# Performance work log

Hardware: AMD Instinct MI355X
Metric: run time of the kernel (lower is better)

Reference implementation:

```python
import jax, jax.numpy as jnp
import numpy as np
from functools import partial

B, S, I, H, L = 32, 512, 512, 512, 2  # batch, seq, input, hidden, layers (bidirectional)


def _uniform(key, shape, k):
    return jax.random.uniform(key, shape, jnp.float32, -k, k)


def setup_inputs() -> dict:
    key = jax.random.key(0)
    keys = jax.random.split(key, 1 + 16)
    inp = {"x": jax.random.normal(keys[0], (B, S, I), jnp.float32)}
    k = 1.0 / H
    ki = 1
    for l in range(L):
        in_sz = I if l == 0 else 2 * H
        for d in ("f", "b"):
            inp[f"w_ih_{l}{d}"] = _uniform(keys[ki], (4 * H, in_sz), k); ki += 1
            inp[f"w_hh_{l}{d}"] = _uniform(keys[ki], (4 * H, H), k); ki += 1
            inp[f"b_ih_{l}{d}"] = _uniform(keys[ki], (4 * H,), k); ki += 1
            inp[f"b_hh_{l}{d}"] = _uniform(keys[ki], (4 * H,), k); ki += 1
    return inp


def _lstm_dir(x_sbi, w_ih, w_hh, b_ih, b_hh, reverse):
    # x_sbi: [S,B,in]. Precompute input projection for all timesteps (one big GEMM).
    xp = jnp.einsum('sbi,gi->sbg', x_sbi, w_ih) + b_ih + b_hh  # [S,B,4H]
    h0 = jnp.zeros((x_sbi.shape[1], H), x_sbi.dtype)
    c0 = jnp.zeros_like(h0)

    def step(carry, xg):
        h, c = carry
        gates = xg + h @ w_hh.T
        i, f, g, o = jnp.split(gates, 4, axis=-1)  # pytorch order i,f,g,o
        i = jax.nn.sigmoid(i); f = jax.nn.sigmoid(f)
        g = jnp.tanh(g); o = jax.nn.sigmoid(o)
        c_new = f * c + i * g
        h_new = o * jnp.tanh(c_new)
        return (h_new, c_new), h_new

    (hT, cT), hs = jax.lax.scan(step, (h0, c0), xp, reverse=reverse)
    return hs, hT, cT  # hs in original time order [S,B,H]


def _forward(x, params):
    seq = jnp.transpose(x, (1, 0, 2))  # [S,B,I]
    final_h, final_c = [], []
    for l in range(L):
        hf, hTf, cTf = _lstm_dir(seq, *params[(l, 'f')], reverse=False)
        hb, hTb, cTb = _lstm_dir(seq, *params[(l, 'b')], reverse=True)
        seq = jnp.concatenate([hf, hb], axis=-1)  # [S,B,2H]
        final_h += [hTf, hTb]; final_c += [cTf, cTb]
    out = jnp.transpose(seq, (1, 0, 2))  # [B,S,2H]
    return out, (jnp.stack(final_h, 0), jnp.stack(final_c, 0))


def reference(x,
              w_ih_0f, w_hh_0f, b_ih_0f, b_hh_0f,
              w_ih_0b, w_hh_0b, b_ih_0b, b_hh_0b,
              w_ih_1f, w_hh_1f, b_ih_1f, b_hh_1f,
              w_ih_1b, w_hh_1b, b_ih_1b, b_hh_1b):
    params = {
        (0, 'f'): (w_ih_0f, w_hh_0f, b_ih_0f, b_hh_0f),
        (0, 'b'): (w_ih_0b, w_hh_0b, b_ih_0b, b_hh_0b),
        (1, 'f'): (w_ih_1f, w_hh_1f, b_ih_1f, b_hh_1f),
        (1, 'b'): (w_ih_1b, w_hh_1b, b_ih_1b, b_hh_1b),
    }
    return _forward(x, params)
```

## Files before the change

### kernel.cpp

```cpp
#include <hip/hip_runtime.h>

#define BB 32
#define SS 512
#define II 512
#define HH 512
#define GG 2048

typedef unsigned short u16;
typedef unsigned int   u32;
typedef unsigned long long u64;

typedef __attribute__((ext_vector_type(8))) short bf16x8;
typedef __attribute__((ext_vector_type(4))) float f32x4;

__device__ __forceinline__ float b2f(u16 h) {
    return __uint_as_float(((u32)h) << 16);
}
__device__ __forceinline__ u16 f2b(float f) {
    u32 u = __float_as_uint(f);
    u32 r = (u + 0x7FFFu + ((u >> 16) & 1u)) >> 16;
    return (u16)r;
}

#ifndef __has_builtin
#define __has_builtin(x) 0
#endif
#if __has_builtin(__builtin_amdgcn_global_load_lds)
#define HAVE_GLL 1
#else
#define HAVE_GLL 0
#endif

typedef __attribute__((address_space(1))) void as1_void;
typedef __attribute__((address_space(3))) void as3_void;

__device__ __forceinline__ void gload16(const void* g, void* l, int lane) {
#if HAVE_GLL
    __builtin_amdgcn_global_load_lds((as1_void*)g, (as3_void*)l, 16, 0, 0);
#else
    *(bf16x8*)((char*)l + lane * 16) = *(const bf16x8*)g;
#endif
}

__global__ void k_convert_x(const float* __restrict__ x, u16* __restrict__ xbf) {
    const int n4 = BB * SS * II / 4;
    for (int e4 = blockIdx.x * blockDim.x + threadIdx.x; e4 < n4;
         e4 += gridDim.x * blockDim.x) {
        int e = e4 * 4;
        int s = e >> 14;
        int b = (e >> 9) & 31;
        int i = e & 511;
        float4 v = *(const float4*)(x + (size_t)b * (SS * II) + (size_t)s * II + i);
        ushort4 o;
        o.x = f2b(v.x); o.y = f2b(v.y); o.z = f2b(v.z); o.w = f2b(v.w);
        *(ushort4*)(xbf + (size_t)s * (BB * II) + (size_t)b * II + i) = o;
    }
}

__global__ void k_cast(const float* __restrict__ src, u16* __restrict__ dst, int n4) {
    for (int e4 = blockIdx.x * blockDim.x + threadIdx.x; e4 < n4;
         e4 += gridDim.x * blockDim.x) {
        float4 v = *(const float4*)(src + (size_t)e4 * 4);
        ushort4 o;
        o.x = f2b(v.x); o.y = f2b(v.y); o.z = f2b(v.z); o.w = f2b(v.w);
        *(ushort4*)(dst + (size_t)e4 * 4) = o;
    }
}

#define BKP 64

__launch_bounds__(256)
__global__ void k_proj(const u16* __restrict__ A,
                       const u16* __restrict__ Wf_, const u16* __restrict__ Wb_,
                       const float* __restrict__ bihf, const float* __restrict__ bhhf,
                       const float* __restrict__ bihb, const float* __restrict__ bhhb,
                       u16* __restrict__ xpf, u16* __restrict__ xpb,
                       int K) {
    const int dir = blockIdx.z;
    const u16* Wm = dir ? Wb_ : Wf_;
    const float* bih = dir ? bihb : bihf;
    const float* bhh = dir ? bhhb : bhhf;
    u16* xp = dir ? xpb : xpf;

    __shared__ __align__(16) u16 As[128 * BKP];
    __shared__ __align__(16) u16 Bs[128 * BKP];

    const int t    = threadIdx.x;
    const int lane = t & 63;
    const int w    = t >> 6;
    const int wm   = w >> 1, wn = w & 1;
    const int m0   = blockIdx.x * 128;
    const int n0   = blockIdx.y * 128;

    f32x4 acc[4][4] = {};

    for (int kt = 0; kt < K; kt += BKP) {
        #pragma unroll
        for (int i = 0; i < 4; ++i) {
            int c   = (w * 4 + i) * 64 + lane;
            int row = c >> 3;
            int lc  = (c & 7) ^ (row & 7);
            int gk  = kt + lc * 8;
            gload16(A  + (size_t)(m0 + row) * K + gk, (char*)As + (w * 4 + i) * 1024, lane);
            gload16(Wm + (size_t)(n0 + row) * K + gk, (char*)Bs + (w * 4 + i) * 1024, lane);
        }
        __syncthreads();

        #pragma unroll
        for (int ks = 0; ks < 2; ++ks) {
            const int kc = ks * 4 + (lane >> 4);
            bf16x8 af[4], bfr[4];
            #pragma unroll
            for (int mi = 0; mi < 4; ++mi) {
                int row = wm * 64 + mi * 16 + (lane & 15);
                af[mi] = *(const bf16x8*)&As[row * BKP + ((kc ^ (row & 7)) << 3)];
            }
            #pragma unroll
            for (int ni = 0; ni < 4; ++ni) {
                int row = wn * 64 + ni * 16 + (lane & 15);
                bfr[ni] = *(const bf16x8*)&Bs[row * BKP + ((kc ^ (row & 7)) << 3)];
            }
            #pragma unroll
            for (int mi = 0; mi < 4; ++mi)
                #pragma unroll
                for (int ni = 0; ni < 4; ++ni)
                    acc[mi][ni] = __builtin_amdgcn_mfma_f32_16x16x32_bf16(
                        af[mi], bfr[ni], acc[mi][ni], 0, 0, 0);
        }
        __syncthreads();
    }

    #pragma unroll
    for (int ni = 0; ni < 4; ++ni) {
        int n = n0 + wn * 64 + ni * 16 + (lane & 15);
        float bias = bih[n] + bhh[n];
        #pragma unroll
        for (int mi = 0; mi < 4; ++mi) {
            #pragma unroll
            for (int r = 0; r < 4; ++r) {
                int m = m0 + wm * 64 + mi * 16 + (lane >> 4) * 4 + r;
                xp[(size_t)m * GG + n] = f2b(acc[mi][ni][r] + bias);
            }
        }
    }
}

__launch_bounds__(256)
__global__ void k_rec(const u16* __restrict__ xpf, const u16* __restrict__ xpb,
                      const float* __restrict__ whf, const float* __restrict__ whb,
                      u64* __restrict__ Hd,
                      u16* __restrict__ hs0,
                      float* __restrict__ out,
                      float* __restrict__ fin,
                      int layer) {
    const int bid  = blockIdx.x;
    const int dir  = bid >> 5;
    const int wg   = bid & 31;
    const int j0   = wg * 16;
    const u16*  xp = dir ? xpb : xpf;
    const float* W = dir ? whb : whf;

    const int t    = threadIdx.x;
    const int lane = t & 63;
    const int g    = t >> 6;

    __shared__ __align__(16) u16 Wfr[64 * 64 * 8];
    __shared__ __align__(16) u16 hl[32 * 512];
    __shared__ float xq[32 * 65];
    __shared__ float gates[4 * 32 * 18];

    for (int it = 0; it < 16; ++it) {
        int task = it * 256 + t;
        int l    = task & 63;
        int blk  = task >> 6;
        int gg   = blk >> 4;
        int kt   = blk & 15;
        const float* src = W + (size_t)(gg * 512 + j0 + (l & 15)) * 512
                             + kt * 32 + (l >> 4) * 8;
        float4 v0 = *(const float4*)src;
        float4 v1 = *(const float4*)(src + 4);
        union { bf16x8 v; u16 a[8]; } u;
        u.a[0] = f2b(v0.x); u.a[1] = f2b(v0.y); u.a[2] = f2b(v0.z); u.a[3] = f2b(v0.w);
        u.a[4] = f2b(v1.x); u.a[5] = f2b(v1.y); u.a[6] = f2b(v1.z); u.a[7] = f2b(v1.w);
        *(bf16x8*)&Wfr[task * 8] = u.v;
    }
    __syncthreads();

    float creg[4] = {0.f, 0.f, 0.f, 0.f};
    const int eb = t >> 2;
    const int ej = t & 3;

    const int sc_c   = t >> 2;
    const int sc_sub = (t & 3) * 4;

    for (int s = 0; s < SS; ++s) {
        const int sa = dir ? (SS - 1 - s) : s;

        if (t < 128) {
            int b = t & 31, gq = t >> 5;
            const u16* xsrc = xp + (size_t)(sa * 32 + b) * GG + gq * 512 + j0;
            bf16x8 v0 = *(const bf16x8*)xsrc;
            bf16x8 v1 = *(const bf16x8*)(xsrc + 8);
            #pragma unroll
            for (int i = 0; i < 8; ++i) {
                xq[b * 65 + gq * 16 + i]     = b2f((u16)v0[i]);
                xq[b * 65 + gq * 16 + 8 + i] = b2f((u16)v1[i]);
            }
        }

        if (s > 0) {
            const u64* Hrd = Hd + ((size_t)((s & 1) * 2 + dir)) * (32 * 256);
            const u32 tgt = (u32)((layer << 10) | s);
            for (;;) {
                u64 w = __hip_atomic_load(Hrd + t, __ATOMIC_RELAXED,
                                          __HIP_MEMORY_SCOPE_AGENT);
                bool f = (((u32)w & 0xffffu) == tgt) &&
                         ((((u32)(w >> 32)) & 0xffffu) == tgt);
                if (__all(f)) break;
            }
            u64 v[32];
            for (;;) {
                #pragma unroll
                for (int i = 0; i < 32; ++i)
                    v[i] = __hip_atomic_load(Hrd + i * 256 + t, __ATOMIC_RELAXED,
                                             __HIP_MEMORY_SCOPE_AGENT);
                bool ok = true;
                #pragma unroll
                for (int i = 0; i < 32; ++i) {
                    ok = ok && (((u32)v[i] & 0xffffu) == tgt);
                    ok = ok && ((((u32)(v[i] >> 32)) & 0xffffu) == tgt);
                }
                if (__all(ok)) break;
            }
            #pragma unroll
            for (int i = 0; i < 32; ++i) {
                u32 two = ((u32)(v[i] >> 16) & 0xffffu) | (((u32)(v[i] >> 48)) << 16);
                int off = i * 1024 + ((sc_c ^ (i & 7)) << 4) + sc_sub;
                *(u32*)((char*)hl + off) = two;
            }
        } else {
            #pragma unroll
            for (int i = 0; i < 32; ++i) {
                int off = i * 1024 + ((sc_c ^ (i & 7)) << 4) + sc_sub;
                *(u32*)((char*)hl + off) = 0u;
            }
        }
        __syncthreads();

        {
            f32x4 acc0 = {0.f, 0.f, 0.f, 0.f}, acc1 = {0.f, 0.f, 0.f, 0.f};
            const int b0 = lane & 15, q = lane >> 4;
            #pragma unroll
            for (int kt = 0; kt < 16; ++kt) {
                int pc = ((kt << 2) + q) ^ (b0 & 7);
                bf16x8 a0 = *(const bf16x8*)&hl[b0 * 512 + pc * 8];
                bf16x8 a1 = *(const bf16x8*)&hl[(b0 + 16) * 512 + pc * 8];
                bf16x8 Bv = *(const bf16x8*)&Wfr[((g * 16 + kt) * 64 + lane) * 8];
                acc0 = __builtin_amdgcn_mfma_f32_16x16x32_bf16(a0, Bv, acc0, 0, 0, 0);
                acc1 = __builtin_amdgcn_mfma_f32_16x16x32_bf16(a1, Bv, acc1, 0, 0, 0);
            }
            #pragma unroll
            for (int r = 0; r < 4; ++r) {
                gates[g * 576 + (q * 4 + r) * 18 + b0]      = acc0[r];
                gates[g * 576 + (16 + q * 4 + r) * 18 + b0] = acc1[r];
            }
        }
        __syncthreads();

        if (t < 128) {
            float hv4[4], cv4[4];
            #pragma unroll
            for (int k = 0; k < 4; ++k) {
                int jj = ej * 4 + k;
                float gi = xq[eb * 65 +      jj] + gates[0 * 576 + eb * 18 + jj];
                float gf = xq[eb * 65 + 16 + jj] + gates[1 * 576 + eb * 18 + jj];
                float gg = xq[eb * 65 + 32 + jj] + gates[2 * 576 + eb * 18 + jj];
                float go = xq[eb * 65 + 48 + jj] + gates[3 * 576 + eb * 18 + jj];
                float ig = 1.f / (1.f + __expf(-gi));
                float fg = 1.f / (1.f + __expf(-gf));
                float gt = tanhf(gg);
                float og = 1.f / (1.f + __expf(-go));
                float c  = fg * creg[k] + ig * gt;
                float h  = og * tanhf(c);
                creg[k] = c; cv4[k] = c; hv4[k] = h;
            }
            u64* Hwr = Hd + ((size_t)(((s + 1) & 1) * 2 + dir)) * (32 * 256);
            const u32 pst = (u32)((layer << 10) | (s + 1));
            u32 w0 = ((u32)f2b(hv4[0]) << 16) | pst;
            u32 w1 = ((u32)f2b(hv4[1]) << 16) | pst;
            u32 w2 = ((u32)f2b(hv4[2]) << 16) | pst;
            u32 w3 = ((u32)f2b(hv4[3]) << 16) | pst;
            u64* dst = Hwr + eb * 256 + ((j0 + ej * 4) >> 1);
            __hip_atomic_store(dst,     (u64)w0 | ((u64)w1 << 32),
                               __ATOMIC_RELAXED, __HIP_MEMORY_SCOPE_AGENT);
            __hip_atomic_store(dst + 1, (u64)w2 | ((u64)w3 << 32),
                               __ATOMIC_RELAXED, __HIP_MEMORY_SCOPE_AGENT);

            union { u64 q; u16 a[4]; } ho;
            #pragma unroll
            for (int k = 0; k < 4; ++k) ho.a[k] = f2b(hv4[k]);
            if (layer == 0) {
                *(u64*)(hs0 + (size_t)sa * (BB * 1024) + (size_t)eb * 1024
                        + dir * 512 + j0 + ej * 4) = ho.q;
            } else {
                *(float4*)(out + (size_t)eb * (SS * 1024) + (size_t)sa * 1024
                           + dir * 512 + j0 + ej * 4) =
                    make_float4(hv4[0], hv4[1], hv4[2], hv4[3]);
            }
            if (s == SS - 1) {
                int sl = layer * 2 + dir;
                *(float4*)(fin + (size_t)sl * (32 * 512) + eb * 512 + j0 + ej * 4) =
                    make_float4(hv4[0], hv4[1], hv4[2], hv4[3]);
                *(float4*)(fin + 65536 + (size_t)sl * (32 * 512) + eb * 512 + j0 + ej * 4) =
                    make_float4(cv4[0], cv4[1], cv4[2], cv4[3]);
            }
        }
        __syncthreads();
    }
}

#define OFF_XBF   ((size_t)0)
#define OFF_HS0   ((size_t)16777216)
#define OFF_XPF   ((size_t)50331648)
#define OFF_XPB   ((size_t)117440512)
#define OFF_WIH0F ((size_t)184549376)
#define OFF_WIH0B ((size_t)186646528)
#define OFF_WIH1F ((size_t)188743680)
#define OFF_WIH1B ((size_t)192937984)
#define OFF_HST   ((size_t)197132288)

extern "C" void kernel_launch(void* const* d_in, const int* in_sizes, int n_in,
                              void* d_out, int out_size, void* d_ws, size_t ws_size,
                              hipStream_t stream) {
    const float* x      = (const float*)d_in[0];
    const float* wih0f  = (const float*)d_in[1];
    const float* whh0f  = (const float*)d_in[2];
    const float* bih0f  = (const float*)d_in[3];
    const float* bhh0f  = (const float*)d_in[4];
    const float* wih0b  = (const float*)d_in[5];
    const float* whh0b  = (const float*)d_in[6];
    const float* bih0b  = (const float*)d_in[7];
    const float* bhh0b  = (const float*)d_in[8];
    const float* wih1f  = (const float*)d_in[9];
    const float* whh1f  = (const float*)d_in[10];
    const float* bih1f  = (const float*)d_in[11];
    const float* bhh1f  = (const float*)d_in[12];
    const float* wih1b  = (const float*)d_in[13];
    const float* whh1b  = (const float*)d_in[14];
    const float* bih1b  = (const float*)d_in[15];
    const float* bhh1b  = (const float*)d_in[16];

    float* out = (float*)d_out;
    char* ws = (char*)d_ws;

    u16* xbf    = (u16*)(ws + OFF_XBF);
    u16* hs0    = (u16*)(ws + OFF_HS0);
    u16* xpf    = (u16*)(ws + OFF_XPF);
    u16* xpb    = (u16*)(ws + OFF_XPB);
    u16* bwih0f = (u16*)(ws + OFF_WIH0F);
    u16* bwih0b = (u16*)(ws + OFF_WIH0B);
    u16* bwih1f = (u16*)(ws + OFF_WIH1F);
    u16* bwih1b = (u16*)(ws + OFF_WIH1B);
    u64* Hd     = (u64*)(ws + OFF_HST);
    float* fin  = out + 16777216;

    k_convert_x<<<1024, 256, 0, stream>>>(x, xbf);
    k_cast<<<512, 256, 0, stream>>>(wih0f, bwih0f, 2048 * 512 / 4);
    k_cast<<<512, 256, 0, stream>>>(wih0b, bwih0b, 2048 * 512 / 4);
    k_cast<<<512, 256, 0, stream>>>(wih1f, bwih1f, 2048 * 1024 / 4);
    k_cast<<<512, 256, 0, stream>>>(wih1b, bwih1b, 2048 * 1024 / 4);

    hipMemsetAsync(ws + OFF_HST, 0, 262144, stream);

    k_proj<<<dim3(128, 16, 2), 256, 0, stream>>>(
        xbf, bwih0f, bwih0b, bih0f, bhh0f, bih0b, bhh0b, xpf, xpb, 512);
    k_rec<<<64, 256, 0, stream>>>(xpf, xpb, whh0f, whh0b, Hd,
                                  hs0, nullptr, fin, 0);

    k_proj<<<dim3(128, 16, 2), 256, 0, stream>>>(
        hs0, bwih1f, bwih1b, bih1f, bhh1f, bih1b, bhh1b, xpf, xpb, 1024);
    k_rec<<<64, 256, 0, stream>>>(xpf, xpb, whh1f, whh1b, Hd,
                                  nullptr, out, fin, 1);
}
```

Before: 5.243 ms.

## Hold recurrent weights in registers and halve recurrence workgroups to 32

```diff
diff --git a/kernel.cpp b/kernel.cpp
--- a/kernel.cpp
+++ b/kernel.cpp
@@ -145,7 +145,7 @@
     }
 }
 
-__launch_bounds__(256)
+__launch_bounds__(256, 1)
 __global__ void k_rec(const u16* __restrict__ xpf, const u16* __restrict__ xpb,
                       const float* __restrict__ whf, const float* __restrict__ whb,
                       u64* __restrict__ Hd,
@@ -154,9 +154,9 @@
                       float* __restrict__ fin,
                       int layer) {
     const int bid  = blockIdx.x;
-    const int dir  = bid >> 5;
-    const int wg   = bid & 31;
-    const int j0   = wg * 16;
+    const int dir  = bid >> 4;
+    const int wg   = bid & 15;
+    const int j0   = wg * 32;
     const u16*  xp = dir ? xpb : xpf;
     const float* W = dir ? whb : whf;
 
@@ -164,31 +164,29 @@
     const int lane = t & 63;
     const int g    = t >> 6;
 
-    __shared__ __align__(16) u16 Wfr[64 * 64 * 8];
     __shared__ __align__(16) u16 hl[32 * 512];
-    __shared__ float xq[32 * 65];
-    __shared__ float gates[4 * 32 * 18];
-
-    for (int it = 0; it < 16; ++it) {
-        int task = it * 256 + t;
-        int l    = task & 63;
-        int blk  = task >> 6;
-        int gg   = blk >> 4;
-        int kt   = blk & 15;
-        const float* src = W + (size_t)(gg * 512 + j0 + (l & 15)) * 512
-                             + kt * 32 + (l >> 4) * 8;
-        float4 v0 = *(const float4*)src;
-        float4 v1 = *(const float4*)(src + 4);
-        union { bf16x8 v; u16 a[8]; } u;
-        u.a[0] = f2b(v0.x); u.a[1] = f2b(v0.y); u.a[2] = f2b(v0.z); u.a[3] = f2b(v0.w);
-        u.a[4] = f2b(v1.x); u.a[5] = f2b(v1.y); u.a[6] = f2b(v1.z); u.a[7] = f2b(v1.w);
-        *(bf16x8*)&Wfr[task * 8] = u.v;
-    }
-    __syncthreads();
+    __shared__ float xq[32 * 129];
+    __shared__ float gates[4 * 32 * 33];
+
+    bf16x8 Bfr[2][16];
+    #pragma unroll
+    for (int nb = 0; nb < 2; ++nb) {
+        #pragma unroll
+        for (int kt = 0; kt < 16; ++kt) {
+            const float* src = W + (size_t)(g * 512 + j0 + nb * 16 + (lane & 15)) * 512
+                                 + kt * 32 + (lane >> 4) * 8;
+            float4 v0 = *(const float4*)src;
+            float4 v1 = *(const float4*)(src + 4);
+            union { bf16x8 v; u16 a[8]; } u;
+            u.a[0] = f2b(v0.x); u.a[1] = f2b(v0.y); u.a[2] = f2b(v0.z); u.a[3] = f2b(v0.w);
+            u.a[4] = f2b(v1.x); u.a[5] = f2b(v1.y); u.a[6] = f2b(v1.z); u.a[7] = f2b(v1.w);
+            Bfr[nb][kt] = u.v;
+        }
+    }
 
     float creg[4] = {0.f, 0.f, 0.f, 0.f};
-    const int eb = t >> 2;
-    const int ej = t & 3;
+    const int eb = t >> 3;
+    const int ec = t & 7;
 
     const int sc_c   = t >> 2;
     const int sc_sub = (t & 3) * 4;
@@ -196,45 +194,43 @@
     for (int s = 0; s < SS; ++s) {
         const int sa = dir ? (SS - 1 - s) : s;
 
-        if (t < 128) {
-            int b = t & 31, gq = t >> 5;
-            const u16* xsrc = xp + (size_t)(sa * 32 + b) * GG + gq * 512 + j0;
+        {
+            int b = t >> 3, seg = t & 7;
+            const u16* xsrc = xp + (size_t)(sa * 32 + b) * GG
+                              + (seg >> 1) * 512 + j0 + (seg & 1) * 16;
             bf16x8 v0 = *(const bf16x8*)xsrc;
             bf16x8 v1 = *(const bf16x8*)(xsrc + 8);
+            float* xdst = &xq[b * 129 + (seg >> 1) * 32 + (seg & 1) * 16];
             #pragma unroll
             for (int i = 0; i < 8; ++i) {
-                xq[b * 65 + gq * 16 + i]     = b2f((u16)v0[i]);
-                xq[b * 65 + gq * 16 + 8 + i] = b2f((u16)v1[i]);
+                xdst[i]     = b2f((u16)v0[i]);
+                xdst[8 + i] = b2f((u16)v1[i]);
             }
         }
 
         if (s > 0) {
             const u64* Hrd = Hd + ((size_t)((s & 1) * 2 + dir)) * (32 * 256);
             const u32 tgt = (u32)((layer << 10) | s);
-            for (;;) {
-                u64 w = __hip_atomic_load(Hrd + t, __ATOMIC_RELAXED,
-                                          __HIP_MEMORY_SCOPE_AGENT);
-                bool f = (((u32)w & 0xffffu) == tgt) &&
-                         ((((u32)(w >> 32)) & 0xffffu) == tgt);
-                if (__all(f)) break;
-            }
             u64 v[32];
+            u32 pend = 0xffffffffu;
             for (;;) {
                 #pragma unroll
-                for (int i = 0; i < 32; ++i)
-                    v[i] = __hip_atomic_load(Hrd + i * 256 + t, __ATOMIC_RELAXED,
-                                             __HIP_MEMORY_SCOPE_AGENT);
-                bool ok = true;
-                #pragma unroll
                 for (int i = 0; i < 32; ++i) {
-                    ok = ok && (((u32)v[i] & 0xffffu) == tgt);
-                    ok = ok && ((((u32)(v[i] >> 32)) & 0xffffu) == tgt);
+                    if (pend & (1u << i)) {
+                        u64 w = __hip_atomic_load(Hrd + i * 256 + t, __ATOMIC_RELAXED,
+                                                  __HIP_MEMORY_SCOPE_AGENT);
+                        if ((((u32)w & 0xffffu) == tgt) &&
+                            (((u32)(w >> 32) & 0xffffu) == tgt)) {
+                            v[i] = w;
+                            pend &= ~(1u << i);
+                        }
+                    }
                 }
-                if (__all(ok)) break;
+                if (__all(pend == 0)) break;
             }
             #pragma unroll
             for (int i = 0; i < 32; ++i) {
-                u32 two = ((u32)(v[i] >> 16) & 0xffffu) | (((u32)(v[i] >> 48)) << 16);
+                u32 two = (u32)((v[i] >> 16) & 0xffffu) | ((u32)(v[i] >> 48) << 16);
                 int off = i * 1024 + ((sc_c ^ (i & 7)) << 4) + sc_sub;
                 *(u32*)((char*)hl + off) = two;
             }
@@ -248,34 +244,43 @@
         __syncthreads();
 
         {
-            f32x4 acc0 = {0.f, 0.f, 0.f, 0.f}, acc1 = {0.f, 0.f, 0.f, 0.f};
+            f32x4 acc[2][2];
+            #pragma unroll
+            for (int mi = 0; mi < 2; ++mi)
+                #pragma unroll
+                for (int nb = 0; nb < 2; ++nb)
+                    acc[mi][nb] = (f32x4){0.f, 0.f, 0.f, 0.f};
             const int b0 = lane & 15, q = lane >> 4;
             #pragma unroll
             for (int kt = 0; kt < 16; ++kt) {
                 int pc = ((kt << 2) + q) ^ (b0 & 7);
                 bf16x8 a0 = *(const bf16x8*)&hl[b0 * 512 + pc * 8];
                 bf16x8 a1 = *(const bf16x8*)&hl[(b0 + 16) * 512 + pc * 8];
-                bf16x8 Bv = *(const bf16x8*)&Wfr[((g * 16 + kt) * 64 + lane) * 8];
-                acc0 = __builtin_amdgcn_mfma_f32_16x16x32_bf16(a0, Bv, acc0, 0, 0, 0);
-                acc1 = __builtin_amdgcn_mfma_f32_16x16x32_bf16(a1, Bv, acc1, 0, 0, 0);
-            }
-            #pragma unroll
-            for (int r = 0; r < 4; ++r) {
-                gates[g * 576 + (q * 4 + r) * 18 + b0]      = acc0[r];
-                gates[g * 576 + (16 + q * 4 + r) * 18 + b0] = acc1[r];
-            }
-        }
-        __syncthreads();
-
-        if (t < 128) {
+                acc[0][0] = __builtin_amdgcn_mfma_f32_16x16x32_bf16(a0, Bfr[0][kt], acc[0][0], 0, 0, 0);
+                acc[0][1] = __builtin_amdgcn_mfma_f32_16x16x32_bf16(a0, Bfr[1][kt], acc[0][1], 0, 0, 0);
+                acc[1][0] = __builtin_amdgcn_mfma_f32_16x16x32_bf16(a1, Bfr[0][kt], acc[1][0], 0, 0, 0);
+                acc[1][1] = __builtin_amdgcn_mfma_f32_16x16x32_bf16(a1, Bfr[1][kt], acc[1][1], 0, 0, 0);
+            }
+            #pragma unroll
+            for (int mi = 0; mi < 2; ++mi)
+                #pragma unroll
+                for (int nb = 0; nb < 2; ++nb)
+                    #pragma unroll
+                    for (int r = 0; r < 4; ++r)
+                        gates[g * 1056 + (mi * 16 + q * 4 + r) * 33 + nb * 16 + b0]
+                            = acc[mi][nb][r];
+        }
+        __syncthreads();
+
+        {
             float hv4[4], cv4[4];
             #pragma unroll
             for (int k = 0; k < 4; ++k) {
-                int jj = ej * 4 + k;
-                float gi = xq[eb * 65 +      jj] + gates[0 * 576 + eb * 18 + jj];
-                float gf = xq[eb * 65 + 16 + jj] + gates[1 * 576 + eb * 18 + jj];
-                float gg = xq[eb * 65 + 32 + jj] + gates[2 * 576 + eb * 18 + jj];
-                float go = xq[eb * 65 + 48 + jj] + gates[3 * 576 + eb * 18 + jj];
+                int jj = ec * 4 + k;
+                float gi = xq[eb * 129 +      jj] + gates[0 * 1056 + eb * 33 + jj];
+                float gf = xq[eb * 129 + 32 + jj] + gates[1 * 1056 + eb * 33 + jj];
+                float gg = xq[eb * 129 + 64 + jj] + gates[2 * 1056 + eb * 33 + jj];
+                float go = xq[eb * 129 + 96 + jj] + gates[3 * 1056 + eb * 33 + jj];
                 float ig = 1.f / (1.f + __expf(-gi));
                 float fg = 1.f / (1.f + __expf(-gf));
                 float gt = tanhf(gg);
@@ -290,7 +295,7 @@
             u32 w1 = ((u32)f2b(hv4[1]) << 16) | pst;
             u32 w2 = ((u32)f2b(hv4[2]) << 16) | pst;
             u32 w3 = ((u32)f2b(hv4[3]) << 16) | pst;
-            u64* dst = Hwr + eb * 256 + ((j0 + ej * 4) >> 1);
+            u64* dst = Hwr + eb * 256 + ((j0 + ec * 4) >> 1);
             __hip_atomic_store(dst,     (u64)w0 | ((u64)w1 << 32),
                                __ATOMIC_RELAXED, __HIP_MEMORY_SCOPE_AGENT);
             __hip_atomic_store(dst + 1, (u64)w2 | ((u64)w3 << 32),
@@ -301,17 +306,17 @@
             for (int k = 0; k < 4; ++k) ho.a[k] = f2b(hv4[k]);
             if (layer == 0) {
                 *(u64*)(hs0 + (size_t)sa * (BB * 1024) + (size_t)eb * 1024
-                        + dir * 512 + j0 + ej * 4) = ho.q;
+                        + dir * 512 + j0 + ec * 4) = ho.q;
             } else {
                 *(float4*)(out + (size_t)eb * (SS * 1024) + (size_t)sa * 1024
-                           + dir * 512 + j0 + ej * 4) =
+                           + dir * 512 + j0 + ec * 4) =
                     make_float4(hv4[0], hv4[1], hv4[2], hv4[3]);
             }
             if (s == SS - 1) {
                 int sl = layer * 2 + dir;
-                *(float4*)(fin + (size_t)sl * (32 * 512) + eb * 512 + j0 + ej * 4) =
+                *(float4*)(fin + (size_t)sl * (32 * 512) + eb * 512 + j0 + ec * 4) =
                     make_float4(hv4[0], hv4[1], hv4[2], hv4[3]);
-                *(float4*)(fin + 65536 + (size_t)sl * (32 * 512) + eb * 512 + j0 + ej * 4) =
+                *(float4*)(fin + 65536 + (size_t)sl * (32 * 512) + eb * 512 + j0 + ec * 4) =
                     make_float4(cv4[0], cv4[1], cv4[2], cv4[3]);
             }
         }
@@ -374,11 +379,11 @@
 
     k_proj<<<dim3(128, 16, 2), 256, 0, stream>>>(
         xbf, bwih0f, bwih0b, bih0f, bhh0f, bih0b, bhh0b, xpf, xpb, 512);
-    k_rec<<<64, 256, 0, stream>>>(xpf, xpb, whh0f, whh0b, Hd,
+    k_rec<<<32, 256, 0, stream>>>(xpf, xpb, whh0f, whh0b, Hd,
                                   hs0, nullptr, fin, 0);
 
     k_proj<<<dim3(128, 16, 2), 256, 0, stream>>>(
         hs0, bwih1f, bwih1b, bih1f, bhh1f, bih1b, bhh1b, xpf, xpb, 1024);
-    k_rec<<<64, 256, 0, stream>>>(xpf, xpb, whh1f, whh1b, Hd,
+    k_rec<<<32, 256, 0, stream>>>(xpf, xpb, whh1f, whh1b, Hd,
                                   nullptr, out, fin, 1);
 }
```

Measured after the change: 12.55 ms. 139% more time.

## Replace step barrier with per-k-tile LDS counters and prefetch hidden state loads

Applied to the files above, without the earlier changes.

```diff
diff --git a/kernel.cpp b/kernel.cpp
--- a/kernel.cpp
+++ b/kernel.cpp
@@ -168,6 +168,7 @@
     __shared__ __align__(16) u16 hl[32 * 512];
     __shared__ float xq[32 * 65];
     __shared__ float gates[4 * 32 * 18];
+    __shared__ u32 ktdone[16];
 
     for (int it = 0; it < 16; ++it) {
         int task = it * 256 + t;
@@ -184,6 +185,7 @@
         u.a[4] = f2b(v1.x); u.a[5] = f2b(v1.y); u.a[6] = f2b(v1.z); u.a[7] = f2b(v1.w);
         *(bf16x8*)&Wfr[task * 8] = u.v;
     }
+    if (t < 16) ktdone[t] = 0u;
     __syncthreads();
 
     float creg[4] = {0.f, 0.f, 0.f, 0.f};
@@ -195,6 +197,16 @@
 
     for (int s = 0; s < SS; ++s) {
         const int sa = dir ? (SS - 1 - s) : s;
+
+        u64 w[32];
+        const u64* Hrd = Hd + ((size_t)((s & 1) * 2 + dir)) * (32 * 256);
+        const u32 tgt = (u32)((layer << 10) | s);
+        if (s > 0) {
+            #pragma unroll
+            for (int i = 0; i < 32; ++i)
+                w[i] = __hip_atomic_load(Hrd + i * 256 + t, __ATOMIC_RELAXED,
+                                         __HIP_MEMORY_SCOPE_AGENT);
+        }
 
         if (t < 128) {
             int b = t & 31, gq = t >> 5;
@@ -209,32 +221,22 @@
         }
 
         if (s > 0) {
-            const u64* Hrd = Hd + ((size_t)((s & 1) * 2 + dir)) * (32 * 256);
-            const u32 tgt = (u32)((layer << 10) | s);
             for (;;) {
-                u64 w = __hip_atomic_load(Hrd + t, __ATOMIC_RELAXED,
-                                          __HIP_MEMORY_SCOPE_AGENT);
-                bool f = (((u32)w & 0xffffu) == tgt) &&
-                         ((((u32)(w >> 32)) & 0xffffu) == tgt);
-                if (__all(f)) break;
-            }
-            u64 v[32];
-            for (;;) {
-                #pragma unroll
-                for (int i = 0; i < 32; ++i)
-                    v[i] = __hip_atomic_load(Hrd + i * 256 + t, __ATOMIC_RELAXED,
-                                             __HIP_MEMORY_SCOPE_AGENT);
                 bool ok = true;
                 #pragma unroll
                 for (int i = 0; i < 32; ++i) {
-                    ok = ok && (((u32)v[i] & 0xffffu) == tgt);
-                    ok = ok && ((((u32)(v[i] >> 32)) & 0xffffu) == tgt);
+                    ok = ok && (((u32)w[i] & 0xffffu) == tgt)
+                            && ((((u32)(w[i] >> 32)) & 0xffffu) == tgt);
                 }
-                if (__all(ok)) break;
+                if (ok) break;
+                #pragma unroll
+                for (int i = 0; i < 32; ++i)
+                    w[i] = __hip_atomic_load(Hrd + i * 256 + t, __ATOMIC_RELAXED,
+                                             __HIP_MEMORY_SCOPE_AGENT);
             }
             #pragma unroll
             for (int i = 0; i < 32; ++i) {
-                u32 two = ((u32)(v[i] >> 16) & 0xffffu) | (((u32)(v[i] >> 48)) << 16);
+                u32 two = (u32)((w[i] >> 16) & 0xffffu) | ((u32)(w[i] >> 48) << 16);
                 int off = i * 1024 + ((sc_c ^ (i & 7)) << 4) + sc_sub;
                 *(u32*)((char*)hl + off) = two;
             }
@@ -245,13 +247,22 @@
                 *(u32*)((char*)hl + off) = 0u;
             }
         }
-        __syncthreads();
+        asm volatile("s_waitcnt lgkmcnt(0)" ::: "memory");
+        atomicAdd(&ktdone[t >> 4], 1u);
 
         {
             f32x4 acc0 = {0.f, 0.f, 0.f, 0.f}, acc1 = {0.f, 0.f, 0.f, 0.f};
             const int b0 = lane & 15, q = lane >> 4;
-            #pragma unroll
-            for (int kt = 0; kt < 16; ++kt) {
+            const u32 kneed = 16u * (u32)(s + 1);
+            #pragma unroll
+            for (int kk = 0; kk < 16; ++kk) {
+                const int kt = (g * 4 + kk) & 15;
+                while (__hip_atomic_load(&ktdone[kt], __ATOMIC_RELAXED,
+                                         __HIP_MEMORY_SCOPE_WORKGROUP) < kneed) {
+                    __builtin_amdgcn_s_sleep(1);
+                }
+                asm volatile("" ::: "memory");
+                __builtin_amdgcn_sched_barrier(0);
                 int pc = ((kt << 2) + q) ^ (b0 & 7);
                 bf16x8 a0 = *(const bf16x8*)&hl[b0 * 512 + pc * 8];
                 bf16x8 a1 = *(const bf16x8*)&hl[(b0 + 16) * 512 + pc * 8];
```

Result: slower. 7.923 ms (+51.1%).

## Double the recurrent workgroup to 512 threads and prefetch next-step hidden state

Applied to the files above, without the earlier changes.

```diff
diff --git a/kernel.cpp b/kernel.cpp
--- a/kernel.cpp
+++ b/kernel.cpp
@@ -145,7 +145,7 @@
     }
 }
 
-__launch_bounds__(256)
+__launch_bounds__(512, 1)
 __global__ void k_rec(const u16* __restrict__ xpf, const u16* __restrict__ xpb,
                       const float* __restrict__ whf, const float* __restrict__ whb,
                       u64* __restrict__ Hd,
@@ -162,15 +162,17 @@
 
     const int t    = threadIdx.x;
     const int lane = t & 63;
-    const int g    = t >> 6;
+    const int wv   = t >> 6;
+    const int g    = wv & 3;
+    const int m    = wv >> 2;
 
     __shared__ __align__(16) u16 Wfr[64 * 64 * 8];
     __shared__ __align__(16) u16 hl[32 * 512];
-    __shared__ float xq[32 * 65];
+    __shared__ float xq[2][32 * 65];
     __shared__ float gates[4 * 32 * 18];
 
-    for (int it = 0; it < 16; ++it) {
-        int task = it * 256 + t;
+    for (int it = 0; it < 8; ++it) {
+        int task = it * 512 + t;
         int l    = task & 63;
         int blk  = task >> 6;
         int gg   = blk >> 4;
@@ -186,136 +188,119 @@
     }
     __syncthreads();
 
-    float creg[4] = {0.f, 0.f, 0.f, 0.f};
-    const int eb = t >> 2;
-    const int ej = t & 3;
-
-    const int sc_c   = t >> 2;
-    const int sc_sub = (t & 3) * 4;
+    const int wd   = t & 255;
+    const int r0   = (t >> 8) * 16;
+    const int sc_c   = wd >> 2;
+    const int sc_sub = (wd & 3) * 4;
+
+    const int eb = t >> 4;
+    const int ej = t & 15;
+    float creg = 0.f;
+
+    u64 w[16];
 
     for (int s = 0; s < SS; ++s) {
         const int sa = dir ? (SS - 1 - s) : s;
 
-        if (t < 128) {
-            int b = t & 31, gq = t >> 5;
-            const u16* xsrc = xp + (size_t)(sa * 32 + b) * GG + gq * 512 + j0;
+        if (t < 256) {
+            int b = t & 31, seg = t >> 5;
+            int gq = seg >> 1, hf = seg & 1;
+            const u16* xsrc = xp + (size_t)(sa * 32 + b) * GG + gq * 512 + j0 + hf * 8;
             bf16x8 v0 = *(const bf16x8*)xsrc;
-            bf16x8 v1 = *(const bf16x8*)(xsrc + 8);
-            #pragma unroll
-            for (int i = 0; i < 8; ++i) {
-                xq[b * 65 + gq * 16 + i]     = b2f((u16)v0[i]);
-                xq[b * 65 + gq * 16 + 8 + i] = b2f((u16)v1[i]);
-            }
+            float* xdst = &xq[s & 1][b * 65 + gq * 16 + hf * 8];
+            #pragma unroll
+            for (int i = 0; i < 8; ++i) xdst[i] = b2f((u16)v0[i]);
         }
 
         if (s > 0) {
             const u64* Hrd = Hd + ((size_t)((s & 1) * 2 + dir)) * (32 * 256);
             const u32 tgt = (u32)((layer << 10) | s);
             for (;;) {
-                u64 w = __hip_atomic_load(Hrd + t, __ATOMIC_RELAXED,
-                                          __HIP_MEMORY_SCOPE_AGENT);
-                bool f = (((u32)w & 0xffffu) == tgt) &&
-                         ((((u32)(w >> 32)) & 0xffffu) == tgt);
-                if (__all(f)) break;
-            }
-            u64 v[32];
-            for (;;) {
-                #pragma unroll
-                for (int i = 0; i < 32; ++i)
-                    v[i] = __hip_atomic_load(Hrd + i * 256 + t, __ATOMIC_RELAXED,
-                                             __HIP_MEMORY_SCOPE_AGENT);
                 bool ok = true;
                 #pragma unroll
-                for (int i = 0; i < 32; ++i) {
-                    ok = ok && (((u32)v[i] & 0xffffu) == tgt);
-                    ok = ok && ((((u32)(v[i] >> 32)) & 0xffffu) == tgt);
+                for (int i = 0; i < 16; ++i) {
+                    ok = ok && (((u32)w[i] & 0xffffu) == tgt)
+                            && ((((u32)(w[i] >> 32)) & 0xffffu) == tgt);
                 }
-                if (__all(ok)) break;
-            }
-            #pragma unroll
-            for (int i = 0; i < 32; ++i) {
-                u32 two = ((u32)(v[i] >> 16) & 0xffffu) | (((u32)(v[i] >> 48)) << 16);
-                int off = i * 1024 + ((sc_c ^ (i & 7)) << 4) + sc_sub;
+                if (ok) break;
+                #pragma unroll
+                for (int i = 0; i < 16; ++i)
+                    w[i] = __hip_atomic_load(Hrd + (r0 + i) * 256 + wd,
+                                             __ATOMIC_RELAXED, __HIP_MEMORY_SCOPE_AGENT);
+            }
+            #pragma unroll
+            for (int i = 0; i < 16; ++i) {
+                int r = r0 + i;
+                u32 two = (u32)((w[i] >> 16) & 0xffffu) | ((u32)(w[i] >> 48) << 16);
+                int off = r * 1024 + ((sc_c ^ (r & 7)) << 4) + sc_sub;
                 *(u32*)((char*)hl + off) = two;
             }
         } else {
             #pragma unroll
-            for (int i = 0; i < 32; ++i) {
-                int off = i * 1024 + ((sc_c ^ (i & 7)) << 4) + sc_sub;
+            for (int i = 0; i < 16; ++i) {
+                int r = r0 + i;
+                int off = r * 1024 + ((sc_c ^ (r & 7)) << 4) + sc_sub;
                 *(u32*)((char*)hl + off) = 0u;
             }
         }
         __syncthreads();
 
         {
-            f32x4 acc0 = {0.f, 0.f, 0.f, 0.f}, acc1 = {0.f, 0.f, 0.f, 0.f};
+            f32x4 acc = {0.f, 0.f, 0.f, 0.f};
             const int b0 = lane & 15, q = lane >> 4;
             #pragma unroll
             for (int kt = 0; kt < 16; ++kt) {
                 int pc = ((kt << 2) + q) ^ (b0 & 7);
-                bf16x8 a0 = *(const bf16x8*)&hl[b0 * 512 + pc * 8];
-                bf16x8 a1 = *(const bf16x8*)&hl[(b0 + 16) * 512 + pc * 8];
+                bf16x8 a0 = *(const bf16x8*)&hl[(b0 + m * 16) * 512 + pc * 8];
                 bf16x8 Bv = *(const bf16x8*)&Wfr[((g * 16 + kt) * 64 + lane) * 8];
-                acc0 = __builtin_amdgcn_mfma_f32_16x16x32_bf16(a0, Bv, acc0, 0, 0, 0);
-                acc1 = __builtin_amdgcn_mfma_f32_16x16x32_bf16(a1, Bv, acc1, 0, 0, 0);
-            }
-            #pragma unroll
-            for (int r = 0; r < 4; ++r) {
-                gates[g * 576 + (q * 4 + r) * 18 + b0]      = acc0[r];
-                gates[g * 576 + (16 + q * 4 + r) * 18 + b0] = acc1[r];
-            }
+                acc = __builtin_amdgcn_mfma_f32_16x16x32_bf16(a0, Bv, acc, 0, 0, 0);
+            }
+            #pragma unroll
+            for (int r = 0; r < 4; ++r)
+                gates[g * 576 + (m * 16 + q * 4 + r) * 18 + b0] = acc[r];
         }
         __syncthreads();
 
-        if (t < 128) {
-            float hv4[4], cv4[4];
-            #pragma unroll
-            for (int k = 0; k < 4; ++k) {
-                int jj = ej * 4 + k;
-                float gi = xq[eb * 65 +      jj] + gates[0 * 576 + eb * 18 + jj];
-                float gf = xq[eb * 65 + 16 + jj] + gates[1 * 576 + eb * 18 + jj];
-                float gg = xq[eb * 65 + 32 + jj] + gates[2 * 576 + eb * 18 + jj];
-                float go = xq[eb * 65 + 48 + jj] + gates[3 * 576 + eb * 18 + jj];
-                float ig = 1.f / (1.f + __expf(-gi));
-                float fg = 1.f / (1.f + __expf(-gf));
-                float gt = tanhf(gg);
-                float og = 1.f / (1.f + __expf(-go));
-                float c  = fg * creg[k] + ig * gt;
-                float h  = og * tanhf(c);
-                creg[k] = c; cv4[k] = c; hv4[k] = h;
-            }
-            u64* Hwr = Hd + ((size_t)(((s + 1) & 1) * 2 + dir)) * (32 * 256);
+        {
+            const float* xrow = &xq[s & 1][eb * 65];
+            float gi = xrow[     ej] + gates[0 * 576 + eb * 18 + ej];
+            float gf = xrow[16 + ej] + gates[1 * 576 + eb * 18 + ej];
+            float gg = xrow[32 + ej] + gates[2 * 576 + eb * 18 + ej];
+            float go = xrow[48 + ej] + gates[3 * 576 + eb * 18 + ej];
+            float ig = 1.f / (1.f + __expf(-gi));
+            float fg = 1.f / (1.f + __expf(-gf));
+            float gt = tanhf(gg);
+            float og = 1.f / (1.f + __expf(-go));
+            float c  = fg * creg + ig * gt;
+            float h  = og * tanhf(c);
+            creg = c;
+
+            u32* Hwr32 = (u32*)(Hd + ((size_t)(((s + 1) & 1) * 2 + dir)) * (32 * 256));
             const u32 pst = (u32)((layer << 10) | (s + 1));
-            u32 w0 = ((u32)f2b(hv4[0]) << 16) | pst;
-            u32 w1 = ((u32)f2b(hv4[1]) << 16) | pst;
-            u32 w2 = ((u32)f2b(hv4[2]) << 16) | pst;
-            u32 w3 = ((u32)f2b(hv4[3]) << 16) | pst;
-            u64* dst = Hwr + eb * 256 + ((j0 + ej * 4) >> 1);
-            __hip_atomic_store(dst,     (u64)w0 | ((u64)w1 << 32),
+            __hip_atomic_store(Hwr32 + eb * 512 + j0 + ej,
+                               ((u32)f2b(h) << 16) | pst,
                                __ATOMIC_RELAXED, __HIP_MEMORY_SCOPE_AGENT);
-            __hip_atomic_store(dst + 1, (u64)w2 | ((u64)w3 << 32),
-                               __ATOMIC_RELAXED, __HIP_MEMORY_SCOPE_AGENT);
-
-            union { u64 q; u16 a[4]; } ho;
-            #pragma unroll
-            for (int k = 0; k < 4; ++k) ho.a[k] = f2b(hv4[k]);
+
+            if (s + 1 < SS) {
+                const u64* Hn = Hd + ((size_t)(((s + 1) & 1) * 2 + dir)) * (32 * 256);
+                #pragma unroll
+                for (int i = 0; i < 16; ++i)
+                    w[i] = __hip_atomic_load(Hn + (r0 + i) * 256 + wd,
+                                             __ATOMIC_RELAXED, __HIP_MEMORY_SCOPE_AGENT);
+            }
+
             if (layer == 0) {
-                *(u64*)(hs0 + (size_t)sa * (BB * 1024) + (size_t)eb * 1024
-                        + dir * 512 + j0 + ej * 4) = ho.q;
+                hs0[(size_t)sa * (BB * 1024) + (size_t)eb * 1024 + dir * 512 + j0 + ej]
+                    = f2b(h);
             } else {
-                *(float4*)(out + (size_t)eb * (SS * 1024) + (size_t)sa * 1024
-                           + dir * 512 + j0 + ej * 4) =
-                    make_float4(hv4[0], hv4[1], hv4[2], hv4[3]);
+                out[(size_t)eb * (SS * 1024) + (size_t)sa * 1024 + dir * 512 + j0 + ej] = h;
             }
             if (s == SS - 1) {
                 int sl = layer * 2 + dir;
-                *(float4*)(fin + (size_t)sl * (32 * 512) + eb * 512 + j0 + ej * 4) =
-                    make_float4(hv4[0], hv4[1], hv4[2], hv4[3]);
-                *(float4*)(fin + 65536 + (size_t)sl * (32 * 512) + eb * 512 + j0 + ej * 4) =
-                    make_float4(cv4[0], cv4[1], cv4[2], cv4[3]);
-            }
-        }
-        __syncthreads();
+                fin[(size_t)sl * (32 * 512) + eb * 512 + j0 + ej] = h;
+                fin[65536 + (size_t)sl * (32 * 512) + eb * 512 + j0 + ej] = c;
+            }
+        }
     }
 }
 
@@ -374,11 +359,11 @@
 
     k_proj<<<dim3(128, 16, 2), 256, 0, stream>>>(
         xbf, bwih0f, bwih0b, bih0f, bhh0f, bih0b, bhh0b, xpf, xpb, 512);
-    k_rec<<<64, 256, 0, stream>>>(xpf, xpb, whh0f, whh0b, Hd,
+    k_rec<<<64, 512, 0, stream>>>(xpf, xpb, whh0f, whh0b, Hd,
                                   hs0, nullptr, fin, 0);
 
     k_proj<<<dim3(128, 16, 2), 256, 0, stream>>>(
         hs0, bwih1f, bwih1b, bih1f, bhh1f, bih1b, bhh1b, xpf, xpb, 1024);
-    k_rec<<<64, 256, 0, stream>>>(xpf, xpb, whh1f, whh1b, Hd,
+    k_rec<<<64, 512, 0, stream>>>(xpf, xpb, whh1f, whh1b, Hd,
                                   nullptr, out, fin, 1);
 }
```

Result: slower. 5.741 ms (+9.5%).
